# Optimization experiments

Measured on AMD Instinct MI355X. Metric: run time of the kernel, lower is better.

Reference implementation:

```python
import jax, jax.numpy as jnp
import numpy as np

B, C, H, W = 4, 192, 56, 56
D_STATE, D_CONV, EXPAND = 16, 3, 2
D_INNER = EXPAND * C
DT_RANK = (C + 15) // 16  # 12


def setup_inputs() -> dict:
    key = jax.random.key(0)
    ks = jax.random.split(key, 16)
    s = 0.02
    return {
        "x": jax.random.normal(ks[0], (B, C, H, W), jnp.float32),
        "ln1_g": jnp.ones((C,), jnp.float32),
        "ln1_b": jnp.zeros((C,), jnp.float32),
        "in_proj_w": jax.random.normal(ks[1], (2 * D_INNER, C), jnp.float32) * s,
        "conv1d_w": jax.random.normal(ks[2], (D_INNER, 1, D_CONV), jnp.float32) * s,
        "conv1d_b": jnp.zeros((D_INNER,), jnp.float32),
        "x_proj_w": jax.random.normal(ks[3], (DT_RANK + 2 * D_STATE, D_INNER), jnp.float32) * s,
        "dt_proj_w": jax.random.normal(ks[4], (D_INNER, DT_RANK), jnp.float32) * (DT_RANK ** -0.5),
        "dt_proj_b": jax.random.uniform(ks[5], (D_INNER,), jnp.float32, -4.6, -2.3),
        "A_log": jnp.tile(jnp.log(jnp.arange(1, D_STATE + 1, dtype=jnp.float32)), (D_INNER, 1)),
        "Dskip": jnp.ones((D_INNER,), jnp.float32),
        "out_proj_w": jax.random.normal(ks[6], (C, D_INNER), jnp.float32) * s,
        "dw_w": jax.random.normal(ks[7], (C, 1, 3, 3), jnp.float32) * s,
        "bn_g": jnp.ones((C,), jnp.float32),
        "bn_b": jnp.zeros((C,), jnp.float32),
        "bn_mean": jax.random.normal(ks[8], (C,), jnp.float32) * 0.1,
        "bn_var": jax.random.uniform(ks[9], (C,), jnp.float32, 0.5, 1.5),
        "ln2_g": jnp.ones((C,), jnp.float32),
        "ln2_b": jnp.zeros((C,), jnp.float32),
        "mlp_w1": jax.random.normal(ks[10], (4 * C, C), jnp.float32) * s,
        "mlp_b1": jnp.zeros((4 * C,), jnp.float32),
        "mlp_w2": jax.random.normal(ks[11], (C, 4 * C), jnp.float32) * s,
        "mlp_b2": jnp.zeros((C,), jnp.float32),
    }


def _ln(x, g, b, eps=1e-5):
    m = jnp.mean(x, -1, keepdims=True)
    v = jnp.var(x, -1, keepdims=True)
    return (x - m) * jax.lax.rsqrt(v + eps) * g + b


def _gelu(x):
    return jax.nn.gelu(x, approximate=False)


def _mamba(xf, in_proj_w, conv1d_w, conv1d_b, x_proj_w, dt_proj_w, dt_proj_b, A_log, Dskip, out_proj_w):
    # xf: (B, L, C) tokens
    Bn, L, _ = xf.shape
    xz = jnp.einsum('blc,ec->ble', xf, in_proj_w)  # (B, L, 2*d_inner)
    xm, z = jnp.split(xz, 2, axis=-1)
    # causal depthwise conv1d over L
    xm_t = jnp.transpose(xm, (0, 2, 1))  # (B, d_inner, L)
    conv = jax.lax.conv_general_dilated(
        xm_t, conv1d_w, (1,), [(D_CONV - 1, 0)],
        feature_group_count=D_INNER,
        dimension_numbers=('NCH', 'OIH', 'NCH'))
    xm = jax.nn.silu(jnp.transpose(conv + conv1d_b[None, :, None], (0, 2, 1)))  # (B, L, d_inner)
    x_dbl = jnp.einsum('bld,ed->ble', xm, x_proj_w)
    dt = x_dbl[..., :DT_RANK]
    Bm = x_dbl[..., DT_RANK:DT_RANK + D_STATE]   # (B, L, n)
    Cm = x_dbl[..., DT_RANK + D_STATE:]          # (B, L, n)
    delta = jax.nn.softplus(jnp.einsum('blr,dr->bld', dt, dt_proj_w) + dt_proj_b)
    A = -jnp.exp(A_log)                           # (d_inner, n)
    deltaA = jnp.exp(delta[..., None] * A)        # (B, L, d, n)
    deltaBx = (delta * xm)[..., None] * Bm[:, :, None, :]  # (B, L, d, n)

    def step(h, inp):
        dA, dBx, Ct = inp
        h = dA * h + dBx                          # (B, d, n)
        y = jnp.einsum('bdn,bn->bd', h, Ct)
        return h, y

    h0 = jnp.zeros((Bn, D_INNER, D_STATE), xm.dtype)
    _, ys = jax.lax.scan(step, h0, (jnp.transpose(deltaA, (1, 0, 2, 3)),
                                    jnp.transpose(deltaBx, (1, 0, 2, 3)),
                                    jnp.transpose(Cm, (1, 0, 2))))
    y = jnp.transpose(ys, (1, 0, 2)) + xm * Dskip  # (B, L, d_inner)
    y = y * jax.nn.silu(z)
    return jnp.einsum('bld,cd->blc', y, out_proj_w)


def reference(x, ln1_g, ln1_b, in_proj_w, conv1d_w, conv1d_b, x_proj_w, dt_proj_w, dt_proj_b,
              A_log, Dskip, out_proj_w, dw_w, bn_g, bn_b, bn_mean, bn_var,
              ln2_g, ln2_b, mlp_w1, mlp_b1, mlp_w2, mlp_b2):
    Bn, Cn, Hn, Wn = x.shape
    # --- branch 1: LN -> SS2D (Mamba over flattened tokens) + skip
    t = jnp.transpose(x, (0, 2, 3, 1))            # (B, H, W, C)
    t = _ln(t, ln1_g, ln1_b)
    tokens = t.reshape(Bn, Hn * Wn, Cn)           # row-major = rearrange 'b c h w -> b (h w) c' after LN
    y = _mamba(tokens, in_proj_w, conv1d_w, conv1d_b, x_proj_w, dt_proj_w, dt_proj_b,
               A_log, Dskip, out_proj_w)
    x1 = x + jnp.transpose(y.reshape(Bn, Hn, Wn, Cn), (0, 3, 1, 2))
    # --- branch 2: depthwise conv -> BN(eval) -> GELU + skip
    dw = jax.lax.conv_general_dilated(x1, dw_w, (1, 1), [(1, 1), (1, 1)],
                                      feature_group_count=Cn,
                                      dimension_numbers=('NCHW', 'OIHW', 'NCHW'))
    bn = (dw - bn_mean[None, :, None, None]) * jax.lax.rsqrt(bn_var + 1e-5)[None, :, None, None]
    bn = bn * bn_g[None, :, None, None] + bn_b[None, :, None, None]
    x2 = x1 + _gelu(bn)
    # --- branch 3: LN -> MLP + skip
    t = jnp.transpose(x2, (0, 2, 3, 1))
    t = _ln(t, ln2_g, ln2_b)
    h = _gelu(jnp.einsum('bhwc,ec->bhwe', t, mlp_w1) + mlp_b1)
    m = jnp.einsum('bhwe,ce->bhwc', h, mlp_w2) + mlp_b2
    return x2 + jnp.transpose(m, (0, 3, 1, 2))
```

## Files before the change

kernel.cpp:

```cpp
#include <hip/hip_runtime.h>
#include <hip/hip_bf16.h>
#include <math.h>

#define BATCH 4
#define CCH   192
#define HH    56
#define WW    56
#define LSEQ  (HH*WW)
#define NTOK  (BATCH*LSEQ)
#define DST   16
#define DIN   384
#define DTR   12
#define XDM   (DTR + 2*DST)
#define NXC   416
#define CL    32
#define NC    (LSEQ/CL)

typedef __attribute__((ext_vector_type(8))) short short8;
typedef __attribute__((ext_vector_type(4))) short short4v;
typedef __attribute__((ext_vector_type(4))) float floatx4;

__device__ __forceinline__ float siluf(float x)  { return x / (1.f + __expf(-x)); }
__device__ __forceinline__ float geluf(float x)  { return 0.5f * x * (1.f + erff(x * 0.70710678118654752f)); }
__device__ __forceinline__ float softplusf(float x) { return (x > 20.f) ? x : log1pf(__expf(x)); }
__device__ __forceinline__ float bf2f(short u) {
    union { unsigned int i; float f; } cv; cv.i = ((unsigned int)(unsigned short)u) << 16; return cv.f;
}
__device__ __forceinline__ short f2bf_bits(float v) {
    __hip_bfloat16 h = __float2bfloat16(v);
    return *(short*)&h;
}

#define WSZ0 147456
#define WSZ2 73728
#define WSZ3 147456
#define WSZ4 147456
__global__ __launch_bounds__(256) void cvt_weights(const float* __restrict__ w0,
                                                   const float* __restrict__ w2, const float* __restrict__ w3,
                                                   const float* __restrict__ w4,
                                                   __hip_bfloat16* __restrict__ o0,
                                                   __hip_bfloat16* __restrict__ o2, __hip_bfloat16* __restrict__ o3,
                                                   __hip_bfloat16* __restrict__ o4) {
    int i = blockIdx.x * 256 + threadIdx.x;
    if (i < WSZ0) { o0[i] = __float2bfloat16(w0[i]); return; } i -= WSZ0;
    if (i < WSZ2) { o2[i] = __float2bfloat16(w2[i]); return; } i -= WSZ2;
    if (i < WSZ3) { o3[i] = __float2bfloat16(w3[i]); return; } i -= WSZ3;
    if (i < WSZ4) { o4[i] = __float2bfloat16(w4[i]); }
}

__global__ __launch_bounds__(256) void make_wcomb(const float* __restrict__ xp_w,
                                                  const float* __restrict__ dt_w,
                                                  __hip_bfloat16* __restrict__ wcomb) {
    int i = blockIdx.x * 256 + threadIdx.x;
    if (i >= NXC * DIN) return;
    int row = i / DIN, k = i % DIN;
    float v;
    if (row < DIN) {
        v = 0.f;
#pragma unroll
        for (int r = 0; r < DTR; r++) v += dt_w[row * DTR + r] * xp_w[r * DIN + k];
    } else {
        v = xp_w[(row - DIN + DTR) * DIN + k];
    }
    wcomb[i] = __float2bfloat16(v);
}

__global__ __launch_bounds__(256) void ln_kernel(const float* __restrict__ x,
                                                 const float* __restrict__ g,
                                                 const float* __restrict__ bta,
                                                 __hip_bfloat16* __restrict__ out) {
    __shared__ float tile[CCH * 65];
    __shared__ float gs[CCH], bs[CCH];
    int t = threadIdx.x;
    int b = blockIdx.y, hw0 = blockIdx.x * 64;
    const float* xb = x + (size_t)b * CCH * LSEQ + hw0;
#pragma unroll 8
    for (int k = 0; k < 48; k++) {
        int idx = k * 256 + t;
        int c = idx >> 6, w = idx & 63;
        tile[c * 65 + w] = xb[(size_t)c * LSEQ + w];
    }
    if (t < CCH) { gs[t] = g[t]; bs[t] = bta[t]; }
    __syncthreads();
    int lane = t & 63, wave = t >> 6;
    int tk = lane & 15, p = lane >> 4;
    int tok = wave * 16 + tk;
    float s = 0.f, s2 = 0.f;
#pragma unroll 8
    for (int i = 0; i < 48; i++) {
        float v = tile[(p * 48 + i) * 65 + tok];
        s += v; s2 += v * v;
    }
    s += __shfl_xor(s, 16); s2 += __shfl_xor(s2, 16);
    s += __shfl_xor(s, 32); s2 += __shfl_xor(s2, 32);
    float mean = s * (1.f / CCH);
    float rstd = rsqrtf(s2 * (1.f / CCH) - mean * mean + 1e-5f);
    int j = lane >> 2, q = lane & 3;
    float mj = __shfl(mean, j);
    float rj = __shfl(rstd, j);
    int wtok = wave * 16 + j;
    __hip_bfloat16* op = out + (size_t)(b * LSEQ + hw0 + wtok) * CCH + q * 48;
#pragma unroll
    for (int kk = 0; kk < 6; kk++) {
        short8 pk;
#pragma unroll
        for (int e = 0; e < 8; e++) {
            int c = q * 48 + kk * 8 + e;
            float v = (tile[c * 65 + wtok] - mj) * rj * gs[c] + bs[c];
            pk[e] = f2bf_bits(v);
        }
        *(short8*)(op + kk * 8) = pk;
    }
}

template<int EPI, typename OutT>
__global__ __launch_bounds__(256) void gemm_mfma(const __hip_bfloat16* __restrict__ A,
                                                 const __hip_bfloat16* __restrict__ W,
                                                 const float* __restrict__ bias,
                                                 const float* __restrict__ res,
                                                 OutT* __restrict__ Cout,
                                                 float* __restrict__ aux,
                                                 int N, int K) {
    __shared__ __align__(16) __hip_bfloat16 As[128 * 40];
    __shared__ __align__(16) __hip_bfloat16 Bs[128 * 40];
    int tid = threadIdx.x;
    int bm = blockIdx.y * 128, bn = blockIdx.x * 128;
    int wave = tid >> 6, lane = tid & 63;
    int wm = (wave >> 1) * 64, wn = (wave & 1) * 64;
    int lm = lane & 15, quad = lane >> 4;
    floatx4 acc[4][4] = {};
    int lrow = tid >> 2;
    int lcol = (tid & 3) * 8;
    for (int k0 = 0; k0 < K; k0 += 32) {
#pragma unroll
        for (int p = 0; p < 2; p++) {
            int row = lrow + p * 64;
            *(short8*)&As[row * 40 + lcol] = *(const short8*)(A + (size_t)(bm + row) * K + k0 + lcol);
            int n = bn + row;
            short8 bv = {0,0,0,0,0,0,0,0};
            if (n < N) bv = *(const short8*)(W + (size_t)n * K + k0 + lcol);
            *(short8*)&Bs[row * 40 + lcol] = bv;
        }
        __syncthreads();
        short8 a[4], b[4];
#pragma unroll
        for (int i = 0; i < 4; i++) a[i] = *(const short8*)&As[(wm + i * 16 + lm) * 40 + quad * 8];
#pragma unroll
        for (int j = 0; j < 4; j++) b[j] = *(const short8*)&Bs[(wn + j * 16 + lm) * 40 + quad * 8];
#pragma unroll
        for (int i = 0; i < 4; i++)
#pragma unroll
            for (int j = 0; j < 4; j++)
                acc[i][j] = __builtin_amdgcn_mfma_f32_16x16x32_bf16(a[i], b[j], acc[i][j], 0, 0, 0);
        __syncthreads();
    }
#pragma unroll
    for (int j = 0; j < 4; j++) {
        int n = bn + wn + j * 16 + lm;
        if (n >= N) continue;
        if (EPI == 5) {
#pragma unroll
            for (int i = 0; i < 4; i++) {
                int mrow = bm + wm + i * 16 + quad * 4;
                if (n < DIN) {
                    float bv = bias[n];
#pragma unroll
                    for (int r = 0; r < 4; r++)
                        Cout[(size_t)(mrow + r) * DIN + n] = (OutT)softplusf(acc[i][j][r] + bv);
                } else {
                    int nb = n - DIN;
#pragma unroll
                    for (int r = 0; r < 4; r++)
                        aux[(size_t)(mrow + r) * 32 + nb] = acc[i][j][r];
                }
            }
            continue;
        }
        float bv = (EPI == 2 || EPI == 4) ? bias[n] : 0.f;
#pragma unroll
        for (int i = 0; i < 4; i++) {
            int mrow = bm + wm + i * 16 + quad * 4;
            if (EPI == 3 || EPI == 4) {
                int bb = mrow / LSEQ;
                int l0 = mrow % LSEQ;
                size_t oidx = ((size_t)(bb * CCH + n)) * LSEQ + l0;
                float4 xr = *(const float4*)(res + oidx);
                float4 v;
                v.x = acc[i][j][0] + bv + xr.x;
                v.y = acc[i][j][1] + bv + xr.y;
                v.z = acc[i][j][2] + bv + xr.z;
                v.w = acc[i][j][3] + bv + xr.w;
                *(float4*)((float*)Cout + oidx) = v;
            } else {
#pragma unroll
                for (int r = 0; r < 4; r++) {
                    float v = acc[i][j][r];
                    if (EPI == 2) { v += bv; v = geluf(v); }
                    Cout[(size_t)(mrow + r) * N + n] = (OutT)v;
                }
            }
        }
    }
}

__global__ __launch_bounds__(256) void conv1d_silu(const __hip_bfloat16* __restrict__ xz,
                                                   const float* __restrict__ w,
                                                   const float* __restrict__ bias,
                                                   __hip_bfloat16* __restrict__ out_bf) {
    int idx = blockIdx.x * 256 + threadIdx.x;
    if (idx >= NTOK * (DIN / 4)) return;
    int m = idx / (DIN / 4), d = (idx % (DIN / 4)) * 4;
    int l = m % LSEQ;
    short4v cur = *(const short4v*)&xz[(size_t)m * (2 * DIN) + d];
    short4v p1 = {0,0,0,0}, p2 = {0,0,0,0};
    if (l >= 1) p1 = *(const short4v*)&xz[(size_t)(m - 1) * (2 * DIN) + d];
    if (l >= 2) p2 = *(const short4v*)&xz[(size_t)(m - 2) * (2 * DIN) + d];
    float4 bv = *(const float4*)&bias[d];
    short4v obv;
#pragma unroll
    for (int jj = 0; jj < 4; jj++) {
        float w0 = w[(d + jj) * 3 + 0], w1 = w[(d + jj) * 3 + 1], w2 = w[(d + jj) * 3 + 2];
        float acc = ((const float*)&bv)[jj] + w2 * bf2f(cur[jj]) + w1 * bf2f(p1[jj]) + w0 * bf2f(p2[jj]);
        obv[jj] = f2bf_bits(siluf(acc));
    }
    *(short4v*)&out_bf[(size_t)m * DIN + d] = obv;
}

__global__ __launch_bounds__(256) void scan_phase1(const __hip_bfloat16* __restrict__ delta,
                                                   const __hip_bfloat16* __restrict__ xm,
                                                   const float* __restrict__ bc,
                                                   const float* __restrict__ A_log,
                                                   float* __restrict__ Pbuf,
                                                   float* __restrict__ Qbuf) {
    __shared__ float b_s[CL][16];
    int t = threadIdx.x;
    int b = blockIdx.z, c = blockIdx.x, d0 = blockIdx.y * 128;
    int m0 = b * LSEQ + c * CL;
    {
        int i = t >> 3, q = (t & 7) * 2;
        *(float2*)&b_s[i][q] = *(const float2*)&bc[(size_t)(m0 + i) * 32 + q];
    }
    __syncthreads();
    int d = d0 + (t >> 1), half = t & 1;
    float An[8];
#pragma unroll
    for (int n4 = 0; n4 < 2; n4++) {
        float4 a = *(const float4*)&A_log[d * DST + half * 8 + n4 * 4];
        An[n4 * 4 + 0] = -__expf(a.x);
        An[n4 * 4 + 1] = -__expf(a.y);
        An[n4 * 4 + 2] = -__expf(a.z);
        An[n4 * 4 + 3] = -__expf(a.w);
    }
    float Q[8];
#pragma unroll
    for (int n = 0; n < 8; n++) Q[n] = 0.f;
    float s = 0.f;
    const __hip_bfloat16* dp = delta + (size_t)m0 * DIN + d;
    const __hip_bfloat16* xp = xm    + (size_t)m0 * DIN + d;
#pragma unroll 4
    for (int i = 0; i < CL; i++) {
        float dlt = bf2f(*(const short*)(dp + (size_t)i * DIN));
        float xv  = bf2f(*(const short*)(xp + (size_t)i * DIN));
        s += dlt;
        float tt = dlt * xv;
#pragma unroll
        for (int n = 0; n < 8; n++) {
            float dA = __expf(dlt * An[n]);
            Q[n] = dA * Q[n] + tt * b_s[i][half * 8 + n];
        }
    }
    size_t o = ((size_t)(b * NC + c) * DIN + d) * DST + half * 8;
#pragma unroll
    for (int n4 = 0; n4 < 2; n4++) {
        float4 Pv, Qv;
        Pv.x = __expf(An[n4 * 4 + 0] * s);
        Pv.y = __expf(An[n4 * 4 + 1] * s);
        Pv.z = __expf(An[n4 * 4 + 2] * s);
        Pv.w = __expf(An[n4 * 4 + 3] * s);
        Qv.x = Q[n4 * 4 + 0]; Qv.y = Q[n4 * 4 + 1];
        Qv.z = Q[n4 * 4 + 2]; Qv.w = Q[n4 * 4 + 3];
        *(float4*)&Pbuf[o + n4 * 4] = Pv;
        *(float4*)&Qbuf[o + n4 * 4] = Qv;
    }
}

__global__ __launch_bounds__(256) void scan_phase2(const float* __restrict__ Pbuf,
                                                   const float* __restrict__ Qbuf,
                                                   float* __restrict__ Hin) {
    int t = blockIdx.x * 256 + threadIdx.x;
    if (t >= BATCH * DIN * DST) return;
    int b = t / (DIN * DST);
    int rem = t % (DIN * DST);
    float h = 0.f;
#pragma unroll 7
    for (int c = 0; c < NC; c++) {
        size_t o = (size_t)(b * NC + c) * (DIN * DST) + rem;
        Hin[o] = h;
        h = Pbuf[o] * h + Qbuf[o];
    }
}

__global__ __launch_bounds__(256) void scan_phase3(const __hip_bfloat16* __restrict__ delta,
                                                   const __hip_bfloat16* __restrict__ xm,
                                                   const float* __restrict__ bc,
                                                   const __hip_bfloat16* __restrict__ xz,
                                                   const float* __restrict__ A_log,
                                                   const float* __restrict__ Dskip,
                                                   const float* __restrict__ Hin,
                                                   __hip_bfloat16* __restrict__ ybuf) {
    __shared__ float bc_s[CL][32];
    int t = threadIdx.x;
    int b = blockIdx.z, c = blockIdx.x, d0 = blockIdx.y * 128;
    int m0 = b * LSEQ + c * CL;
    {
        int i = t >> 3, q = (t & 7) * 4;
        *(float4*)&bc_s[i][q] = *(const float4*)&bc[(size_t)(m0 + i) * 32 + q];
    }
    __syncthreads();
    int d = d0 + (t >> 1), half = t & 1;
    float An[8];
#pragma unroll
    for (int n4 = 0; n4 < 2; n4++) {
        float4 a = *(const float4*)&A_log[d * DST + half * 8 + n4 * 4];
        An[n4 * 4 + 0] = -__expf(a.x);
        An[n4 * 4 + 1] = -__expf(a.y);
        An[n4 * 4 + 2] = -__expf(a.z);
        An[n4 * 4 + 3] = -__expf(a.w);
    }
    float h[8];
    size_t o = ((size_t)(b * NC + c) * DIN + d) * DST + half * 8;
    {
        float4 h0 = *(const float4*)&Hin[o];
        float4 h1 = *(const float4*)&Hin[o + 4];
        h[0] = h0.x; h[1] = h0.y; h[2] = h0.z; h[3] = h0.w;
        h[4] = h1.x; h[5] = h1.y; h[6] = h1.z; h[7] = h1.w;
    }
    float Dv = Dskip[d];
    const __hip_bfloat16* dp = delta + (size_t)m0 * DIN + d;
    const __hip_bfloat16* xp = xm    + (size_t)m0 * DIN + d;
    const __hip_bfloat16* zp = xz + (size_t)m0 * (2 * DIN) + DIN + d;
    __hip_bfloat16* yo = ybuf + (size_t)m0 * DIN + d;
#pragma unroll 2
    for (int i = 0; i < CL; i++) {
        float dlt = bf2f(*(const short*)(dp + (size_t)i * DIN));
        float xv  = bf2f(*(const short*)(xp + (size_t)i * DIN));
        float tt = dlt * xv;
        float y = 0.f;
#pragma unroll
        for (int n = 0; n < 8; n++) {
            float dA = __expf(dlt * An[n]);
            h[n] = dA * h[n] + tt * bc_s[i][half * 8 + n];
            y += h[n] * bc_s[i][16 + half * 8 + n];
        }
        y += __shfl_xor(y, 1);
        if (half == 0) {
            float zv = bf2f(*(const short*)(zp + (size_t)i * (2 * DIN)));
            yo[(size_t)i * DIN] = __float2bfloat16((y + xv * Dv) * siluf(zv));
        }
    }
}

__global__ __launch_bounds__(256) void dwconv_bn_gelu(const float* __restrict__ x1,
                                                      const float* __restrict__ wdw,
                                                      const float* __restrict__ bn_g,
                                                      const float* __restrict__ bn_b,
                                                      const float* __restrict__ bn_mean,
                                                      const float* __restrict__ bn_var,
                                                      float* __restrict__ x2) {
    int idx = blockIdx.x * 256 + threadIdx.x;
    if (idx >= NTOK * CCH / 4) return;
    int w4 = idx % (WW / 4); int tmp = idx / (WW / 4);
    int h = tmp % HH; tmp /= HH;
    int c = tmp % CCH; int b = tmp / CCH;
    int w0 = w4 * 4;
    const float* base = x1 + ((size_t)(b * CCH + c)) * LSEQ;
    float acc[4] = {0.f, 0.f, 0.f, 0.f};
    float4 mid0;
#pragma unroll
    for (int dh = -1; dh <= 1; dh++) {
        int hh = h + dh;
        if (hh < 0 || hh >= HH) { if (dh == 0) mid0 = *(const float4*)&base[h * WW + w0]; continue; }
        const float* row = base + hh * WW;
        float4 mid = *(const float4*)&row[w0];
        if (dh == 0) mid0 = mid;
        float lft = (w0 > 0) ? row[w0 - 1] : 0.f;
        float rgt = (w0 + 4 < WW) ? row[w0 + 4] : 0.f;
        float wA = wdw[c * 9 + (dh + 1) * 3 + 0];
        float wB = wdw[c * 9 + (dh + 1) * 3 + 1];
        float wC = wdw[c * 9 + (dh + 1) * 3 + 2];
        float in0 = lft, in1 = mid.x, in2 = mid.y, in3 = mid.z, in4 = mid.w, in5 = rgt;
        acc[0] += wA * in0 + wB * in1 + wC * in2;
        acc[1] += wA * in1 + wB * in2 + wC * in3;
        acc[2] += wA * in2 + wB * in3 + wC * in4;
        acc[3] += wA * in3 + wB * in4 + wC * in5;
    }
    float mu = bn_mean[c], rv = rsqrtf(bn_var[c] + 1e-5f) * bn_g[c], bb = bn_b[c];
    float4 o;
    o.x = mid0.x + geluf((acc[0] - mu) * rv + bb);
    o.y = mid0.y + geluf((acc[1] - mu) * rv + bb);
    o.z = mid0.z + geluf((acc[2] - mu) * rv + bb);
    o.w = mid0.w + geluf((acc[3] - mu) * rv + bb);
    *(float4*)&x2[((size_t)(b * CCH + c)) * LSEQ + h * WW + w0] = o;
}

extern "C" void kernel_launch(void* const* d_in, const int* in_sizes, int n_in,
                              void* d_out, int out_size, void* d_ws, size_t ws_size,
                              hipStream_t stream) {
    const float* x         = (const float*)d_in[0];
    const float* ln1_g     = (const float*)d_in[1];
    const float* ln1_b     = (const float*)d_in[2];
    const float* in_proj_w = (const float*)d_in[3];
    const float* conv_w    = (const float*)d_in[4];
    const float* conv_b    = (const float*)d_in[5];
    const float* x_proj_w  = (const float*)d_in[6];
    const float* dt_proj_w = (const float*)d_in[7];
    const float* dt_proj_b = (const float*)d_in[8];
    const float* A_log     = (const float*)d_in[9];
    const float* Dskip     = (const float*)d_in[10];
    const float* out_proj_w= (const float*)d_in[11];
    const float* dw_w      = (const float*)d_in[12];
    const float* bn_g      = (const float*)d_in[13];
    const float* bn_b      = (const float*)d_in[14];
    const float* bn_mean   = (const float*)d_in[15];
    const float* bn_var    = (const float*)d_in[16];
    const float* ln2_g     = (const float*)d_in[17];
    const float* ln2_b     = (const float*)d_in[18];
    const float* mlp_w1    = (const float*)d_in[19];
    const float* mlp_b1    = (const float*)d_in[20];
    const float* mlp_w2    = (const float*)d_in[21];
    const float* mlp_b2    = (const float*)d_in[22];
    float* out = (float*)d_out;

    char* wsb = (char*)d_ws;
    __hip_bfloat16* xz_bf     = (__hip_bfloat16*)wsb;                 wsb += (size_t)NTOK * 768 * 2;
    __hip_bfloat16* xm_bf     = (__hip_bfloat16*)wsb;                 wsb += (size_t)NTOK * DIN * 2;
    __hip_bfloat16* delta_bf  = (__hip_bfloat16*)wsb;                 wsb += (size_t)NTOK * DIN * 2;
    float*          bc        = (float*)wsb;                          wsb += (size_t)NTOK * 32 * 4;
    float*          Pbuf      = (float*)wsb;                          wsb += (size_t)NTOK * 192 * 4;
    float*          Qbuf      = (float*)wsb;                          wsb += (size_t)NTOK * 192 * 4;
    float*          Hin       = (float*)wsb;                          wsb += (size_t)NTOK * 192 * 4;
    float*          x1        = (float*)wsb;                          wsb += (size_t)NTOK * CCH * 4;
    float*          x2        = (float*)wsb;                          wsb += (size_t)NTOK * CCH * 4;
    __hip_bfloat16* tokens_bf = (__hip_bfloat16*)wsb;                 wsb += (size_t)NTOK * CCH * 2;
    __hip_bfloat16* ybuf_bf   = (__hip_bfloat16*)wsb;                 wsb += (size_t)NTOK * DIN * 2;
    __hip_bfloat16* hidden_bf = (__hip_bfloat16*)wsb;                 wsb += (size_t)NTOK * 768 * 2;
    __hip_bfloat16* in_w_bf   = (__hip_bfloat16*)wsb;                 wsb += WSZ0 * 2;
    __hip_bfloat16* op_w_bf   = (__hip_bfloat16*)wsb;                 wsb += WSZ2 * 2;
    __hip_bfloat16* w1_bf     = (__hip_bfloat16*)wsb;                 wsb += WSZ3 * 2;
    __hip_bfloat16* w2_bf     = (__hip_bfloat16*)wsb;                 wsb += WSZ4 * 2;
    __hip_bfloat16* wcomb_bf  = (__hip_bfloat16*)wsb;                 wsb += (size_t)NXC * DIN * 2;

    cvt_weights<<<(WSZ0 + WSZ2 + WSZ3 + WSZ4 + 255) / 256, 256, 0, stream>>>(
        in_proj_w, out_proj_w, mlp_w1, mlp_w2, in_w_bf, op_w_bf, w1_bf, w2_bf);
    make_wcomb<<<(NXC * DIN + 255) / 256, 256, 0, stream>>>(x_proj_w, dt_proj_w, wcomb_bf);
    ln_kernel<<<dim3(LSEQ / 64, BATCH), 256, 0, stream>>>(x, ln1_g, ln1_b, tokens_bf);
    gemm_mfma<0, __hip_bfloat16><<<dim3(768 / 128, NTOK / 128), 256, 0, stream>>>(tokens_bf, in_w_bf, nullptr, nullptr, xz_bf, nullptr, 768, CCH);
    conv1d_silu<<<(NTOK * (DIN / 4) + 255) / 256, 256, 0, stream>>>(xz_bf, conv_w, conv_b, xm_bf);
    gemm_mfma<5, __hip_bfloat16><<<dim3(4, NTOK / 128), 256, 0, stream>>>(xm_bf, wcomb_bf, dt_proj_b, nullptr, delta_bf, bc, NXC, DIN);
    scan_phase1<<<dim3(NC, DIN / 128, BATCH), 256, 0, stream>>>(delta_bf, xm_bf, bc, A_log, Pbuf, Qbuf);
    scan_phase2<<<(BATCH * DIN * DST + 255) / 256, 256, 0, stream>>>(Pbuf, Qbuf, Hin);
    scan_phase3<<<dim3(NC, DIN / 128, BATCH), 256, 0, stream>>>(delta_bf, xm_bf, bc, xz_bf, A_log, Dskip, Hin, ybuf_bf);
    gemm_mfma<3, float><<<dim3(2, NTOK / 128), 256, 0, stream>>>(ybuf_bf, op_w_bf, nullptr, x, x1, nullptr, CCH, DIN);
    dwconv_bn_gelu<<<(NTOK * CCH / 4 + 255) / 256, 256, 0, stream>>>(x1, dw_w, bn_g, bn_b, bn_mean, bn_var, x2);
    ln_kernel<<<dim3(LSEQ / 64, BATCH), 256, 0, stream>>>(x2, ln2_g, ln2_b, tokens_bf);
    gemm_mfma<2, __hip_bfloat16><<<dim3(768 / 128, NTOK / 128), 256, 0, stream>>>(tokens_bf, w1_bf, mlp_b1, nullptr, hidden_bf, nullptr, 768, CCH);
    gemm_mfma<4, float><<<dim3(2, NTOK / 128), 256, 0, stream>>>(hidden_bf, w2_bf, mlp_b2, x2, out, nullptr, CCH, 4 * CCH);
}
```

Before: 326.8 us.

## Double-buffer GEMM shared tiles and stage bf16 epilogue through LDS

The MFMA GEMM now prefetches the next K-slice into registers while computing on the current shared-memory buffer, and writes it into a second buffer, which halves the barriers per K step and hides global load latency. The non-residual epilogues (GELU, softplus, plain) now write bf16 results into a per-wave LDS tile and then emit coalesced 16-byte row stores instead of scattered 2-byte stores. Shared memory doubles, which may lower occupancy. The staged path assumes bf16 output and full tiles in N for those epilogues.

```diff
diff --git a/kernel.cpp b/kernel.cpp
--- a/kernel.cpp
+++ b/kernel.cpp
@@ -11,7 +11,6 @@
 #define DST   16
 #define DIN   384
 #define DTR   12
-#define XDM   (DTR + 2*DST)
 #define NXC   416
 #define CL    32
 #define NC    (LSEQ/CL)
@@ -121,8 +120,7 @@
                                                  OutT* __restrict__ Cout,
                                                  float* __restrict__ aux,
                                                  int N, int K) {
-    __shared__ __align__(16) __hip_bfloat16 As[128 * 40];
-    __shared__ __align__(16) __hip_bfloat16 Bs[128 * 40];
+    __shared__ __align__(16) __hip_bfloat16 AsBs[2][2][128 * 40];
     int tid = threadIdx.x;
     int bm = blockIdx.y * 128, bn = blockIdx.x * 128;
     int wave = tid >> 6, lane = tid & 63;
@@ -131,56 +129,60 @@
     floatx4 acc[4][4] = {};
     int lrow = tid >> 2;
     int lcol = (tid & 3) * 8;
-    for (int k0 = 0; k0 < K; k0 += 32) {
-#pragma unroll
-        for (int p = 0; p < 2; p++) {
-            int row = lrow + p * 64;
-            *(short8*)&As[row * 40 + lcol] = *(const short8*)(A + (size_t)(bm + row) * K + k0 + lcol);
-            int n = bn + row;
-            short8 bv = {0,0,0,0,0,0,0,0};
-            if (n < N) bv = *(const short8*)(W + (size_t)n * K + k0 + lcol);
-            *(short8*)&Bs[row * 40 + lcol] = bv;
-        }
-        __syncthreads();
+    const int nk = K >> 5;
+    short8 zero8 = {0,0,0,0,0,0,0,0};
+    short8 ra0, ra1, rb0, rb1;
+    ra0 = *(const short8*)(A + (size_t)(bm + lrow) * K + lcol);
+    ra1 = *(const short8*)(A + (size_t)(bm + lrow + 64) * K + lcol);
+    {
+        int n0 = bn + lrow, n1 = bn + lrow + 64;
+        rb0 = (n0 < N) ? *(const short8*)(W + (size_t)n0 * K + lcol) : zero8;
+        rb1 = (n1 < N) ? *(const short8*)(W + (size_t)n1 * K + lcol) : zero8;
+    }
+    *(short8*)&AsBs[0][0][lrow * 40 + lcol] = ra0;
+    *(short8*)&AsBs[0][0][(lrow + 64) * 40 + lcol] = ra1;
+    *(short8*)&AsBs[0][1][lrow * 40 + lcol] = rb0;
+    *(short8*)&AsBs[0][1][(lrow + 64) * 40 + lcol] = rb1;
+    __syncthreads();
+    for (int kk = 0; kk < nk; kk++) {
+        int cur = kk & 1;
+        bool more = (kk + 1 < nk);
+        if (more) {
+            int k0 = (kk + 1) * 32;
+            ra0 = *(const short8*)(A + (size_t)(bm + lrow) * K + k0 + lcol);
+            ra1 = *(const short8*)(A + (size_t)(bm + lrow + 64) * K + k0 + lcol);
+            int n0 = bn + lrow, n1 = bn + lrow + 64;
+            rb0 = (n0 < N) ? *(const short8*)(W + (size_t)n0 * K + k0 + lcol) : zero8;
+            rb1 = (n1 < N) ? *(const short8*)(W + (size_t)n1 * K + k0 + lcol) : zero8;
+        }
         short8 a[4], b[4];
 #pragma unroll
-        for (int i = 0; i < 4; i++) a[i] = *(const short8*)&As[(wm + i * 16 + lm) * 40 + quad * 8];
-#pragma unroll
-        for (int j = 0; j < 4; j++) b[j] = *(const short8*)&Bs[(wn + j * 16 + lm) * 40 + quad * 8];
+        for (int i = 0; i < 4; i++) a[i] = *(const short8*)&AsBs[cur][0][(wm + i * 16 + lm) * 40 + quad * 8];
+#pragma unroll
+        for (int j = 0; j < 4; j++) b[j] = *(const short8*)&AsBs[cur][1][(wn + j * 16 + lm) * 40 + quad * 8];
 #pragma unroll
         for (int i = 0; i < 4; i++)
 #pragma unroll
             for (int j = 0; j < 4; j++)
                 acc[i][j] = __builtin_amdgcn_mfma_f32_16x16x32_bf16(a[i], b[j], acc[i][j], 0, 0, 0);
+        if (more) {
+            int nxt = cur ^ 1;
+            *(short8*)&AsBs[nxt][0][lrow * 40 + lcol] = ra0;
+            *(short8*)&AsBs[nxt][0][(lrow + 64) * 40 + lcol] = ra1;
+            *(short8*)&AsBs[nxt][1][lrow * 40 + lcol] = rb0;
+            *(short8*)&AsBs[nxt][1][(lrow + 64) * 40 + lcol] = rb1;
+        }
         __syncthreads();
     }
-#pragma unroll
-    for (int j = 0; j < 4; j++) {
-        int n = bn + wn + j * 16 + lm;
-        if (n >= N) continue;
-        if (EPI == 5) {
+    if constexpr (EPI == 3 || EPI == 4) {
+#pragma unroll
+        for (int j = 0; j < 4; j++) {
+            int n = bn + wn + j * 16 + lm;
+            if (n >= N) continue;
+            float bv = (EPI == 4) ? bias[n] : 0.f;
 #pragma unroll
             for (int i = 0; i < 4; i++) {
                 int mrow = bm + wm + i * 16 + quad * 4;
-                if (n < DIN) {
-                    float bv = bias[n];
-#pragma unroll
-                    for (int r = 0; r < 4; r++)
-                        Cout[(size_t)(mrow + r) * DIN + n] = (OutT)softplusf(acc[i][j][r] + bv);
-                } else {
-                    int nb = n - DIN;
-#pragma unroll
-                    for (int r = 0; r < 4; r++)
-                        aux[(size_t)(mrow + r) * 32 + nb] = acc[i][j][r];
-                }
-            }
-            continue;
-        }
-        float bv = (EPI == 2 || EPI == 4) ? bias[n] : 0.f;
-#pragma unroll
-        for (int i = 0; i < 4; i++) {
-            int mrow = bm + wm + i * 16 + quad * 4;
-            if (EPI == 3 || EPI == 4) {
                 int bb = mrow / LSEQ;
                 int l0 = mrow % LSEQ;
                 size_t oidx = ((size_t)(bb * CCH + n)) * LSEQ + l0;
@@ -191,12 +193,55 @@
                 v.z = acc[i][j][2] + bv + xr.z;
                 v.w = acc[i][j][3] + bv + xr.w;
                 *(float4*)((float*)Cout + oidx) = v;
-            } else {
-#pragma unroll
-                for (int r = 0; r < 4; r++) {
-                    float v = acc[i][j][r];
-                    if (EPI == 2) { v += bv; v = geluf(v); }
-                    Cout[(size_t)(mrow + r) * N + n] = (OutT)v;
+            }
+        }
+        return;
+    } else {
+        __hip_bfloat16* tb = ((__hip_bfloat16*)&AsBs[0][0][0]) + wave * (64 * 72);
+        bool has_tile = (EPI != 5) || (bn < DIN);
+        if (has_tile) {
+#pragma unroll
+            for (int j = 0; j < 4; j++) {
+                int n = bn + wn + j * 16 + lm;
+                float bv = (EPI == 2 || EPI == 5) ? bias[n] : 0.f;
+#pragma unroll
+                for (int i = 0; i < 4; i++) {
+#pragma unroll
+                    for (int r = 0; r < 4; r++) {
+                        float v = acc[i][j][r];
+                        if (EPI == 2) v = geluf(v + bv);
+                        if (EPI == 5) v = softplusf(v + bv);
+                        tb[(i * 16 + quad * 4 + r) * 72 + j * 16 + lm] = __float2bfloat16(v);
+                    }
+                }
+            }
+        }
+        __syncthreads();
+        if (has_tile) {
+            int ldc = (EPI == 5) ? DIN : N;
+            int srow = lane >> 3, schunk = lane & 7;
+            __hip_bfloat16* cb = (__hip_bfloat16*)Cout;
+#pragma unroll
+            for (int pass = 0; pass < 8; pass++) {
+                int row = pass * 8 + srow;
+                short8 v = *(const short8*)&tb[row * 72 + schunk * 8];
+                *(short8*)(cb + (size_t)(bm + wm + row) * ldc + bn + wn + schunk * 8) = v;
+            }
+        }
+        if constexpr (EPI == 5) {
+            if (bn >= DIN) {
+#pragma unroll
+                for (int j = 0; j < 4; j++) {
+                    int n = bn + wn + j * 16 + lm;
+                    if (n >= N) continue;
+                    int nb = n - DIN;
+#pragma unroll
+                    for (int i = 0; i < 4; i++) {
+                        int mrow = bm + wm + i * 16 + quad * 4;
+#pragma unroll
+                        for (int r = 0; r < 4; r++)
+                            aux[(size_t)(mrow + r) * 32 + nb] = acc[i][j][r];
+                    }
                 }
             }
         }
```

Result: faster. 310.3 us (-5.0%).
